# Kernel optimization log

Hardware: AMD Instinct MI355X
Metric: run time of the kernel (lower is better)

The kernel has to match this reference:

```python
import jax, jax.numpy as jnp
import numpy as np

B, S, D, L, H = 4, 2048, 1024, 2, 8  # batch, seq, d_model, hierarchy levels, heads
DH = D // H


def _ln(x, g, b, eps=1e-5):
    mu = jnp.mean(x, axis=-1, keepdims=True)
    xc = x - mu
    var = jnp.mean(xc * xc, axis=-1, keepdims=True)
    return xc * jax.lax.rsqrt(var + eps) * g + b


def setup_inputs() -> dict:
    key = jax.random.key(0)
    ks = jax.random.split(key, 16)
    s = 0.02
    f32 = jnp.float32
    return {
        "x": jax.random.normal(ks[0], (B, S, D), f32),
        "hierarchy_levels": jax.random.randint(ks[1], (B, S), 0, 3),
        # per-level processor MLPs (stacked over level axis)
        "p1_w": jax.random.normal(ks[2], (L, D, D), f32) * s,
        "p1_b": jnp.zeros((L, D), f32),
        "p2_w": jax.random.normal(ks[3], (L, D, D), f32) * s,
        "p2_b": jnp.zeros((L, D), f32),
        "ln_g": jnp.ones((L, D), f32),
        "ln_b": jnp.zeros((L, D), f32),
        # multihead attention projections
        "wq": jax.random.normal(ks[4], (D, D), f32) * s,
        "bq": jnp.zeros((D,), f32),
        "wk": jax.random.normal(ks[5], (D, D), f32) * s,
        "bk": jnp.zeros((D,), f32),
        "wv": jax.random.normal(ks[6], (D, D), f32) * s,
        "bv": jnp.zeros((D,), f32),
        "wo": jax.random.normal(ks[7], (D, D), f32) * s,
        "bo": jnp.zeros((D,), f32),
        # integration MLP: Linear(L*D -> D), SiLU, Linear(D -> D), LayerNorm
        "i1_w": jax.random.normal(ks[8], (L * D, D), f32) * s,
        "i1_b": jnp.zeros((D,), f32),
        "i2_w": jax.random.normal(ks[9], (D, D), f32) * s,
        "i2_b": jnp.zeros((D,), f32),
        "iln_g": jnp.ones((D,), f32),
        "iln_b": jnp.zeros((D,), f32),
    }


def reference(x, hierarchy_levels, p1_w, p1_b, p2_w, p2_b, ln_g, ln_b,
              wq, bq, wk, bk, wv, bv, wo, bo,
              i1_w, i1_b, i2_w, i2_b, iln_g, iln_b):
    # --- per-token expert routing: compute all L processors, select by level ---
    t = jax.nn.silu(jnp.einsum('bsd,lde->lbse', x, p1_w) + p1_b[:, None, None, :])
    h = jnp.einsum('lbse,led->lbsd', t, p2_w) + p2_b[:, None, None, :]
    h = _ln(h, ln_g[:, None, None, :], ln_b[:, None, None, :])  # [L,B,S,D]
    oh = jax.nn.one_hot(hierarchy_levels, L, dtype=x.dtype)      # [B,S,L]; level>=L -> all-zero row
    hsel = jnp.einsum('lbsd,bsl->bsd', h, oh)                    # [B,S,D]
    # --- self-attention over routed outputs ---
    q = (hsel @ wq + bq).reshape(B, S, H, DH)
    k = (hsel @ wk + bk).reshape(B, S, H, DH)
    v = (hsel @ wv + bv).reshape(B, S, H, DH)
    scores = jnp.einsum('bqhd,bkhd->bhqk', q, k) / np.sqrt(DH).astype(x.dtype)
    a = jax.nn.softmax(scores, axis=-1)                          # [B,H,S,S]
    ctx = jnp.einsum('bhqk,bkhd->bqhd', a, v).reshape(B, S, D)
    attended = ctx @ wo + bo
    attn_weights = jnp.mean(a, axis=1)                           # torch avg over heads: [B,S,S]
    # --- integration MLP ---
    z = jnp.concatenate([hsel, attended], axis=-1)               # [B,S,2D]
    z = jax.nn.silu(z @ i1_w + i1_b) @ i2_w + i2_b
    out = _ln(z, iln_g, iln_b)
    return out, attn_weights
```

## Files before the change

### kernel.cpp

```cpp
#include <hip/hip_runtime.h>
#include <cstdint>
#include <cstddef>

#define B_ 4
#define S_ 2048
#define D_ 1024
#define H_ 8
#define DH_ 128
#define MTOT 8192
#define NT_ 32
#define SCALE2 (0.08838834764831845f * 1.4426950408889634f)

typedef __attribute__((ext_vector_type(8))) short s16x8;
typedef __attribute__((ext_vector_type(4))) float f32x4;
typedef __attribute__((ext_vector_type(8))) __bf16 bf16x8;

static __device__ __forceinline__ f32x4 mfma16(s16x8 a, s16x8 b, f32x4 c) {
  return __builtin_amdgcn_mfma_f32_16x16x32_bf16(
      __builtin_bit_cast(bf16x8, a), __builtin_bit_cast(bf16x8, b), c, 0, 0, 0);
}
static __device__ __forceinline__ unsigned short f2bf(float f) {
  unsigned u = __builtin_bit_cast(unsigned, f);
  u += 0x7fffu + ((u >> 16) & 1u);
  return (unsigned short)(u >> 16);
}
static __device__ __forceinline__ float bf2f(unsigned short u) {
  return __builtin_bit_cast(float, (unsigned)u << 16);
}
static __device__ __forceinline__ unsigned cvtpk2(float a, float b) {
  unsigned r;
  asm("v_cvt_pk_bf16_f32 %0, %1, %2" : "=v"(r) : "v"(a), "v"(b));
  return r;
}
static __device__ __forceinline__ void gload_lds16(const void* g, void* l) {
  __builtin_amdgcn_global_load_lds(
      (__attribute__((address_space(1))) void*)(void*)(g),
      (__attribute__((address_space(3))) void*)(l), 16, 0, 0);
}

__global__ __launch_bounds__(256) void xconv_kernel(const float* __restrict__ x,
                                                    unsigned short* __restrict__ xb) {
  long i = ((long)blockIdx.x * 256 + threadIdx.x) * 4;
  float4 v = *(const float4*)(x + i);
  ushort4 o;
  o.x = f2bf(v.x); o.y = f2bf(v.y); o.z = f2bf(v.z); o.w = f2bf(v.w);
  *(ushort4*)(xb + i) = o;
}

__global__ __launch_bounds__(256) void route_kernel(const int* __restrict__ levels,
                                                    int* __restrict__ cnt,
                                                    int* __restrict__ ridx,
                                                    int* __restrict__ act,
                                                    int* __restrict__ act2) {
  const int row = blockIdx.x * 256 + threadIdx.x;
  const int lane = threadIdx.x & 63;
  const int lvl = levels[row];
  const unsigned long long lmlt = (lane == 63) ? ~0ULL >> 1 : (1ULL << lane) - 1;

#pragma unroll
  for (int c = 0; c < 2; c++) {
    bool pred = (lvl == c);
    unsigned long long mask = __ballot(pred);
    int total = __popcll(mask);
    if (total) {
      int leader = __ffsll((long long)mask) - 1;
      int base = 0;
      if (lane == leader) base = atomicAdd(&cnt[c], total);
      base = __shfl(base, leader);
      if (pred) ridx[c * MTOT + base + __popcll(mask & lmlt)] = row;
    }
  }
  {
    bool pred = (lvl < 2);
    unsigned long long mask = __ballot(pred);
    int total = __popcll(mask);
    if (total) {
      int leader = __ffsll((long long)mask) - 1;
      int base = 0;
      if (lane == leader) base = atomicAdd(&cnt[2], total);
      base = __shfl(base, leader);
      if (pred) act[base + __popcll(mask & lmlt)] = row;
    }
    unsigned long long mask2 = ~mask;
    int total2 = 64 - total;
    if (total2) {
      int leader2 = __ffsll((long long)mask2) - 1;
      int base2 = 0;
      if (lane == leader2) base2 = atomicAdd(&cnt[3], total2);
      base2 = __shfl(base2, leader2);
      if (!pred) act2[base2 + __popcll(mask2 & lmlt)] = row;
    }
  }
}

__global__ __launch_bounds__(256) void lvl2fill_kernel(
    const int* __restrict__ act2, const int* __restrict__ cntp,
    const float* __restrict__ bq, const float* __restrict__ bk,
    const float* __restrict__ bv,
    unsigned short* __restrict__ qb, unsigned short* __restrict__ kb,
    unsigned short* __restrict__ vb, unsigned short* __restrict__ z) {
  const int idx = blockIdx.x;
  if (idx >= *cntp) return;
  const long row = act2[idx];
  const int t = threadIdx.x;
  const float4 q4 = *(const float4*)(bq + t * 4);
  const float4 k4 = *(const float4*)(bk + t * 4);
  const float4 v4 = *(const float4*)(bv + t * 4);
  ushort4 qo, ko, vo;
  qo.x = f2bf(q4.x * SCALE2); qo.y = f2bf(q4.y * SCALE2);
  qo.z = f2bf(q4.z * SCALE2); qo.w = f2bf(q4.w * SCALE2);
  ko.x = f2bf(k4.x); ko.y = f2bf(k4.y); ko.z = f2bf(k4.z); ko.w = f2bf(k4.w);
  vo.x = f2bf(v4.x); vo.y = f2bf(v4.y); vo.z = f2bf(v4.z); vo.w = f2bf(v4.w);
  *(ushort4*)(qb + row * 1024 + t * 4) = qo;
  *(ushort4*)(kb + row * 1024 + t * 4) = ko;
  *(ushort4*)(vb + row * 1024 + t * 4) = vo;
  *(ushort4*)(z + row * 2048 + t * 4) = (ushort4){0, 0, 0, 0};
}

struct WtDesc { const float* src; unsigned short* dst; long dst_ld; long dst_off; };
struct WtArgs { WtDesc d[10]; };
__global__ __launch_bounds__(256) void wtrans_all_kernel(WtArgs a) {
  __shared__ unsigned short tile[32][33];
  const int wi = blockIdx.y >> 5;
  const WtDesc de = a.d[wi];
  int r0 = (blockIdx.y & 31) * 32, c0 = blockIdx.x * 32;
  int tr = threadIdx.x >> 5, tc = threadIdx.x & 31;
#pragma unroll
  for (int i = 0; i < 4; i++)
    tile[tr + i * 8][tc] = f2bf(de.src[(long)(r0 + tr + i * 8) * 1024 + c0 + tc]);
  __syncthreads();
#pragma unroll
  for (int i = 0; i < 4; i++)
    de.dst[(long)(c0 + tr + i * 8) * de.dst_ld + de.dst_off + r0 + tc] = tile[tc][tr + i * 8];
}

__global__ __launch_bounds__(256) void vtrans_kernel(const unsigned short* __restrict__ V,
                                                     unsigned short* __restrict__ Vt) {
  __shared__ unsigned short tile[32][33];
  int b = blockIdx.z;
  int h = blockIdx.y >> 2, d0 = (blockIdx.y & 3) * 32;
  int s0 = blockIdx.x * 32;
  int tr = threadIdx.x >> 5, tc = threadIdx.x & 31;
#pragma unroll
  for (int i = 0; i < 4; i++)
    tile[tr + i * 8][tc] = V[((long)(b * S_) + s0 + tr + i * 8) * D_ + h * DH_ + d0 + tc];
  __syncthreads();
  const int sk = s0 + tc;
  const int k6 = sk & 63;
  const int slot = ((k6 >> 5) << 5) | (((k6 >> 2) & 3) << 3) | (((k6 >> 4) & 1) << 2) | (k6 & 3);
  const int ss = (sk & ~63) | slot;
#pragma unroll
  for (int i = 0; i < 4; i++)
    Vt[((long)(b * H_ + h) * DH_ + d0 + tr + i * 8) * S_ + ss] = tile[tc][tr + i * 8];
}

template <int TAG>
__global__ __launch_bounds__(256) void gemm_kernel(
    const unsigned short* __restrict__ A, int lda,
    const unsigned short* __restrict__ Wt, int ldw,
    const float* __restrict__ bias, float oscale,
    unsigned short* __restrict__ Cb, float* __restrict__ Cf, int ldc,
    int K, int do_silu) {
  __shared__ unsigned short lA[128 * 64];
  __shared__ unsigned short lB[128 * 64];
  const int t = threadIdx.x;
  const int wid = t >> 6, lane = t & 63;
  const int g = lane >> 4, lc = lane & 15;
  const int wr = wid >> 1, wc = wid & 1;
  const int nwg = gridDim.x * gridDim.y;
  int flat = blockIdx.x + gridDim.x * blockIdx.y;
  flat = (flat & 7) * (nwg >> 3) + (flat >> 3);
  const int m0 = (flat / gridDim.x) * 128;
  const int n0 = (flat % gridDim.x) * 128;
  const int srow = lane >> 3, scol = lane & 7;
  const int sxor = (scol ^ srow) << 4;

  f32x4 acc[4][4];
#pragma unroll
  for (int i = 0; i < 4; i++)
#pragma unroll
    for (int j = 0; j < 4; j++) acc[i][j] = (f32x4){0.f, 0.f, 0.f, 0.f};

  const int nk = K >> 6;
  for (int kt = 0; kt < nk; ++kt) {
    const int k0 = kt << 6;
#pragma unroll
    for (int i = 0; i < 4; i++) {
      const int r0 = wid * 32 + i * 8;
      gload_lds16((const char*)(A + (m0 + r0 + srow) * (long)lda + k0) + sxor,
                  (char*)lA + r0 * 128);
      gload_lds16((const char*)(Wt + (n0 + r0 + srow) * (long)ldw + k0) + sxor,
                  (char*)lB + r0 * 128);
    }
    __syncthreads();
#pragma unroll
    for (int kk = 0; kk < 2; kk++) {
      s16x8 af[4], bfr[4];
#pragma unroll
      for (int i = 0; i < 4; i++) {
        int row = wr * 64 + i * 16 + lc;
        af[i] = *(const s16x8*)((const char*)lA + row * 128 +
                                ((kk * 64 + g * 16) ^ ((row & 7) << 4)));
      }
#pragma unroll
      for (int j = 0; j < 4; j++) {
        int row = wc * 64 + j * 16 + lc;
        bfr[j] = *(const s16x8*)((const char*)lB + row * 128 +
                                 ((kk * 64 + g * 16) ^ ((row & 7) << 4)));
      }
#pragma unroll
      for (int i = 0; i < 4; i++)
#pragma unroll
        for (int j = 0; j < 4; j++) acc[i][j] = mfma16(af[i], bfr[j], acc[i][j]);
    }
    __syncthreads();
  }
#pragma unroll
  for (int i = 0; i < 4; i++) {
    const long rbase = m0 + wr * 64 + i * 16 + g * 4;
#pragma unroll
    for (int j = 0; j < 4; j++) {
      const int col = n0 + wc * 64 + j * 16 + lc;
      const float bv = bias[col];
#pragma unroll
      for (int r = 0; r < 4; r++) {
        float v = (acc[i][j][r] + bv) * oscale;
        if (do_silu) v = v / (1.f + __expf(-v));
        if (Cb) Cb[(rbase + r) * (long)ldc + col] = f2bf(v);
        else Cf[(rbase + r) * (long)ldc + col] = v;
      }
    }
  }
}

template <int TAG>
__global__ __launch_bounds__(512) void gemm8_kernel(
    const unsigned short* __restrict__ A, int lda,
    const unsigned short* __restrict__ Wt, int ldw,
    const float* __restrict__ bias, float oscale,
    unsigned short* __restrict__ Cb, int ldc,
    int K, int do_silu) {
  __shared__ unsigned short lA[128 * 64];
  __shared__ unsigned short lB[128 * 64];
  const int t = threadIdx.x;
  const int wid = t >> 6, lane = t & 63;
  const int g = lane >> 4, lc = lane & 15;
  const int wr = wid >> 1, wc = wid & 1;
  const int nwg = gridDim.x * gridDim.y;
  int flat = blockIdx.x + gridDim.x * blockIdx.y;
  flat = (flat & 7) * (nwg >> 3) + (flat >> 3);
  const int m0 = (flat / gridDim.x) * 128;
  const int n0 = (flat % gridDim.x) * 128;
  const int srow = lane >> 3, scol = lane & 7;
  const int sxor = (scol ^ srow) << 4;

  f32x4 acc[2][4];
#pragma unroll
  for (int i = 0; i < 2; i++)
#pragma unroll
    for (int j = 0; j < 4; j++) acc[i][j] = (f32x4){0.f, 0.f, 0.f, 0.f};

  const int nk = K >> 6;
  for (int kt = 0; kt < nk; ++kt) {
    const int k0 = kt << 6;
#pragma unroll
    for (int i = 0; i < 2; i++) {
      const int r0 = wid * 16 + i * 8;
      gload_lds16((const char*)(A + (m0 + r0 + srow) * (long)lda + k0) + sxor,
                  (char*)lA + r0 * 128);
      gload_lds16((const char*)(Wt + (n0 + r0 + srow) * (long)ldw + k0) + sxor,
                  (char*)lB + r0 * 128);
    }
    __syncthreads();
#pragma unroll
    for (int kk = 0; kk < 2; kk++) {
      s16x8 af[2], bfr[4];
#pragma unroll
      for (int i = 0; i < 2; i++) {
        int row = wr * 32 + i * 16 + lc;
        af[i] = *(const s16x8*)((const char*)lA + row * 128 +
                                ((kk * 64 + g * 16) ^ ((row & 7) << 4)));
      }
#pragma unroll
      for (int j = 0; j < 4; j++) {
        int row = wc * 64 + j * 16 + lc;
        bfr[j] = *(const s16x8*)((const char*)lB + row * 128 +
                                 ((kk * 64 + g * 16) ^ ((row & 7) << 4)));
      }
#pragma unroll
      for (int i = 0; i < 2; i++)
#pragma unroll
        for (int j = 0; j < 4; j++) acc[i][j] = mfma16(af[i], bfr[j], acc[i][j]);
    }
    __syncthreads();
  }
#pragma unroll
  for (int i = 0; i < 2; i++) {
    const long rbase = m0 + wr * 32 + i * 16 + g * 4;
#pragma unroll
    for (int j = 0; j < 4; j++) {
      const int col = n0 + wc * 64 + j * 16 + lc;
      const float bv = bias[col];
#pragma unroll
      for (int r = 0; r < 4; r++) {
        float v = (acc[i][j][r] + bv) * oscale;
        if (do_silu) v = v / (1.f + __expf(-v));
        Cb[(rbase + r) * (long)ldc + col] = f2bf(v);
      }
    }
  }
}

template <int RMAP>
__global__ __launch_bounds__(512) void gemm8_moe_kernel(
    const unsigned short* __restrict__ A, int lda,
    const unsigned short* __restrict__ Wt0, int ldw,
    const float* __restrict__ bias0,
    unsigned short* __restrict__ Cb, int ldc,
    int K, int do_silu, const int* __restrict__ ridx, const int* __restrict__ cnt2) {
  __shared__ unsigned short lA[128 * 64];
  __shared__ unsigned short lB[128 * 64];
  const int t = threadIdx.x;
  const int wid = t >> 6, lane = t & 63;
  const int g = lane >> 4, lc = lane & 15;
  const int wr = wid >> 1, wc = wid & 1;
  const int nwg = gridDim.x * gridDim.y;
  int flat = blockIdx.x + gridDim.x * blockIdx.y;
  flat = (flat & 7) * (nwg >> 3) + (flat >> 3);
  const int m0 = (flat / gridDim.x) * 128;
  const int n0 = (flat % gridDim.x) * 128;
  const int lvl = m0 >> 12;
  const int lm0 = m0 & 4095;
  if (lm0 >= cnt2[lvl]) return;
  const unsigned short* Wt = Wt0 + (long)lvl * 1048576;
  const float* bias = bias0 + lvl * 1024;
  const int srow = lane >> 3, scol = lane & 7;
  const int sxor = (scol ^ srow) << 4;

  const unsigned short* abase[2];
#pragma unroll
  for (int i = 0; i < 2; i++) {
    int ar;
    if (RMAP) ar = ridx[lvl * MTOT + lm0 + wid * 16 + i * 8 + srow];
    else ar = m0 + wid * 16 + i * 8 + srow;
    abase[i] = A + (long)ar * lda;
  }

  f32x4 acc[2][4];
#pragma unroll
  for (int i = 0; i < 2; i++)
#pragma unroll
    for (int j = 0; j < 4; j++) acc[i][j] = (f32x4){0.f, 0.f, 0.f, 0.f};

  const int nk = K >> 6;
  for (int kt = 0; kt < nk; ++kt) {
    const int k0 = kt << 6;
#pragma unroll
    for (int i = 0; i < 2; i++) {
      const int r0 = wid * 16 + i * 8;
      gload_lds16((const char*)(abase[i] + k0) + sxor, (char*)lA + r0 * 128);
      gload_lds16((const char*)(Wt + (n0 + r0 + srow) * (long)ldw + k0) + sxor,
                  (char*)lB + r0 * 128);
    }
    __syncthreads();
#pragma unroll
    for (int kk = 0; kk < 2; kk++) {
      s16x8 af[2], bfr[4];
#pragma unroll
      for (int i = 0; i < 2; i++) {
        int row = wr * 32 + i * 16 + lc;
        af[i] = *(const s16x8*)((const char*)lA + row * 128 +
                                ((kk * 64 + g * 16) ^ ((row & 7) << 4)));
      }
#pragma unroll
      for (int j = 0; j < 4; j++) {
        int row = wc * 64 + j * 16 + lc;
        bfr[j] = *(const s16x8*)((const char*)lB + row * 128 +
                                 ((kk * 64 + g * 16) ^ ((row & 7) << 4)));
      }
#pragma unroll
      for (int i = 0; i < 2; i++)
#pragma unroll
        for (int j = 0; j < 4; j++) acc[i][j] = mfma16(af[i], bfr[j], acc[i][j]);
    }
    __syncthreads();
  }
#pragma unroll
  for (int i = 0; i < 2; i++) {
    const long rbase = m0 + wr * 32 + i * 16 + g * 4;
#pragma unroll
    for (int j = 0; j < 4; j++) {
      const int col = n0 + wc * 64 + j * 16 + lc;
      const float bv = bias[col];
#pragma unroll
      for (int r = 0; r < 4; r++) {
        float v = acc[i][j][r] + bv;
        if (do_silu) v = v / (1.f + __expf(-v));
        Cb[(rbase + r) * (long)ldc + col] = f2bf(v);
      }
    }
  }
}

__global__ __launch_bounds__(256) void wct_gemm_kernel(
    const unsigned short* __restrict__ A,
    const unsigned short* __restrict__ Wb,
    float* __restrict__ Cf) {
  __shared__ unsigned short lA[128 * 64];
  __shared__ unsigned short lB[128 * 64];
  const int t = threadIdx.x;
  const int wid = t >> 6, lane = t & 63;
  const int g = lane >> 4, lc = lane & 15;
  const int wr = wid >> 1, wc = wid & 1;
  const int chunk = blockIdx.y >> 3;
  const int m0 = (blockIdx.y & 7) * 128;
  const int n0 = blockIdx.x * 128;
  const unsigned short* A0 = A + chunk * 256;
  const unsigned short* W0 = Wb + chunk * 256;
  float* C0 = Cf + (long)chunk * 1048576;
  const int srow = lane >> 3, scol = lane & 7;
  const int sxor = (scol ^ srow) << 4;

  f32x4 acc[4][4];
#pragma unroll
  for (int i = 0; i < 4; i++)
#pragma unroll
    for (int j = 0; j < 4; j++) acc[i][j] = (f32x4){0.f, 0.f, 0.f, 0.f};

  for (int kt = 0; kt < 4; ++kt) {
    const int k0 = kt << 6;
#pragma unroll
    for (int i = 0; i < 4; i++) {
      const int r0 = wid * 32 + i * 8;
      gload_lds16((const char*)(A0 + (m0 + r0 + srow) * 2048L + k0) + sxor,
                  (char*)lA + r0 * 128);
      gload_lds16((const char*)(W0 + (n0 + r0 + srow) * 1024L + k0) + sxor,
                  (char*)lB + r0 * 128);
    }
    __syncthreads();
#pragma unroll
    for (int kk = 0; kk < 2; kk++) {
      s16x8 af[4], bfr[4];
#pragma unroll
      for (int i = 0; i < 4; i++) {
        int row = wr * 64 + i * 16 + lc;
        af[i] = *(const s16x8*)((const char*)lA + row * 128 +
                                ((kk * 64 + g * 16) ^ ((row & 7) << 4)));
      }
#pragma unroll
      for (int j = 0; j < 4; j++) {
        int row = wc * 64 + j * 16 + lc;
        bfr[j] = *(const s16x8*)((const char*)lB + row * 128 +
                                 ((kk * 64 + g * 16) ^ ((row & 7) << 4)));
      }
#pragma unroll
      for (int i = 0; i < 4; i++)
#pragma unroll
        for (int j = 0; j < 4; j++) acc[i][j] = mfma16(af[i], bfr[j], acc[i][j]);
    }
    __syncthreads();
  }
#pragma unroll
  for (int i = 0; i < 4; i++) {
    const long rbase = m0 + wr * 64 + i * 16 + g * 4;
#pragma unroll
    for (int j = 0; j < 4; j++) {
      const int col = n0 + wc * 64 + j * 16 + lc;
#pragma unroll
      for (int r = 0; r < 4; r++) C0[(rbase + r) * 1024L + col] = acc[i][j][r];
    }
  }
}

__global__ __launch_bounds__(256) void wct_reduce_kernel(
    const float* __restrict__ hraw, unsigned short* __restrict__ i1t) {
  long e = ((long)blockIdx.x * 256 + threadIdx.x) * 2;
  float a0 = hraw[e] + hraw[e + 1048576] + hraw[e + 2097152] + hraw[e + 3145728];
  float a1 = hraw[e + 1] + hraw[e + 1 + 1048576] + hraw[e + 1 + 2097152] +
             hraw[e + 1 + 3145728];
  unsigned pk = cvtpk2(a0, a1);
  long n = e >> 10, c = e & 1023;
  *(unsigned*)(i1t + n * 2048 + 1024 + c) = pk;
}

__global__ __launch_bounds__(256) void biascomb_kernel(
    const unsigned short* __restrict__ i1t, const float* __restrict__ bo,
    const float* __restrict__ i1b, float* __restrict__ bias_c) {
  const int n = blockIdx.x, t = threadIdx.x;
  ushort4 w = *(const ushort4*)(i1t + (long)n * 2048 + 1024 + t * 4);
  float4 b = *(const float4*)(bo + t * 4);
  float s = bf2f(w.x) * b.x + bf2f(w.y) * b.y + bf2f(w.z) * b.z + bf2f(w.w) * b.w;
#pragma unroll
  for (int m = 32; m; m >>= 1) s += __shfl_xor(s, m);
  __shared__ float ws_[4];
  if ((t & 63) == 0) ws_[t >> 6] = s;
  __syncthreads();
  if (t == 0) bias_c[n] = i1b[n] + ws_[0] + ws_[1] + ws_[2] + ws_[3];
}

__global__ __launch_bounds__(256) void ln_moe_kernel(
    const unsigned short* __restrict__ in, const int* __restrict__ ridx,
    const int* __restrict__ cnt2,
    const float* __restrict__ gg0, const float* __restrict__ bb0,
    unsigned short* __restrict__ outb, long ldo) {
  const int row = blockIdx.x;
  const int lvl = row >> 12;
  const int lrow = row & 4095;
  if (lrow >= cnt2[lvl]) return;
  const int orow = ridx[lvl * MTOT + lrow];
  const float* gg = gg0 + lvl * 1024;
  const float* bb = bb0 + lvl * 1024;
  const int t = threadIdx.x;
  const ushort4 u = *(const ushort4*)(in + (long)row * D_ + t * 4);
  float v0 = bf2f(u.x), v1 = bf2f(u.y), v2 = bf2f(u.z), v3 = bf2f(u.w);
  float s1 = v0 + v1 + v2 + v3;
  float s2 = v0 * v0 + v1 * v1 + v2 * v2 + v3 * v3;
#pragma unroll
  for (int m = 32; m; m >>= 1) {
    s1 += __shfl_xor(s1, m);
    s2 += __shfl_xor(s2, m);
  }
  __shared__ float w1[4], w2[4];
  if ((t & 63) == 0) { w1[t >> 6] = s1; w2[t >> 6] = s2; }
  __syncthreads();
  s1 = w1[0] + w1[1] + w1[2] + w1[3];
  s2 = w2[0] + w2[1] + w2[2] + w2[3];
  const float mu = s1 * (1.f / D_);
  const float var = s2 * (1.f / D_) - mu * mu;
  const float rs = rsqrtf(var + 1e-5f);
  float vv[4] = {v0, v1, v2, v3};
#pragma unroll
  for (int jj = 0; jj < 4; jj++) {
    int col = t * 4 + jj;
    float y = (vv[jj] - mu) * rs * gg[col] + bb[col];
    outb[(long)orow * ldo + col] = f2bf(y);
  }
}

__global__ __launch_bounds__(256) void ln_kernel(
    const unsigned short* __restrict__ in,
    const float* __restrict__ gg, const float* __restrict__ bb,
    float* __restrict__ outf) {
  const int row = blockIdx.x;
  const int t = threadIdx.x;
  const ushort4 u = *(const ushort4*)(in + (long)row * D_ + t * 4);
  float v0 = bf2f(u.x), v1 = bf2f(u.y), v2 = bf2f(u.z), v3 = bf2f(u.w);
  float s1 = v0 + v1 + v2 + v3;
  float s2 = v0 * v0 + v1 * v1 + v2 * v2 + v3 * v3;
#pragma unroll
  for (int m = 32; m; m >>= 1) {
    s1 += __shfl_xor(s1, m);
    s2 += __shfl_xor(s2, m);
  }
  __shared__ float w1[4], w2[4];
  if ((t & 63) == 0) { w1[t >> 6] = s1; w2[t >> 6] = s2; }
  __syncthreads();
  s1 = w1[0] + w1[1] + w1[2] + w1[3];
  s2 = w2[0] + w2[1] + w2[2] + w2[3];
  const float mu = s1 * (1.f / D_);
  const float var = s2 * (1.f / D_) - mu * mu;
  const float rs = rsqrtf(var + 1e-5f);
  float vv[4] = {v0, v1, v2, v3};
#pragma unroll
  for (int jj = 0; jj < 4; jj++) {
    int col = t * 4 + jj;
    outf[(long)row * D_ + col] = (vv[jj] - mu) * rs * gg[col] + bb[col];
  }
}

__global__ __launch_bounds__(256) void gemm_qkv_kernel(
    const unsigned short* __restrict__ A, int lda,
    const unsigned short* __restrict__ Wt,
    const float* __restrict__ bq, const float* __restrict__ bk,
    const float* __restrict__ bv,
    unsigned short* __restrict__ qb, unsigned short* __restrict__ kb,
    unsigned short* __restrict__ vb,
    const int* __restrict__ act, const int* __restrict__ cntp) {
  __shared__ unsigned short lA[128 * 64];
  __shared__ unsigned short lB[128 * 64];
  const int t = threadIdx.x;
  const int wid = t >> 6, lane = t & 63;
  const int g = lane >> 4, lc = lane & 15;
  const int wr = wid >> 1, wc = wid & 1;
  const int nwg = gridDim.x * gridDim.y;
  int flat = blockIdx.x + gridDim.x * blockIdx.y;
  flat = (flat & 7) * (nwg >> 3) + (flat >> 3);
  const int m0 = (flat / gridDim.x) * 128;
  const int n0 = (flat % gridDim.x) * 128;
  if (m0 >= *cntp) return;
  const int srow = lane >> 3, scol = lane & 7;
  const int sxor = (scol ^ srow) << 4;

  const unsigned short* abase[4];
#pragma unroll
  for (int i = 0; i < 4; i++)
    abase[i] = A + (long)act[m0 + wid * 32 + i * 8 + srow] * lda;

  f32x4 acc[4][4];
#pragma unroll
  for (int i = 0; i < 4; i++)
#pragma unroll
    for (int j = 0; j < 4; j++) acc[i][j] = (f32x4){0.f, 0.f, 0.f, 0.f};

  for (int kt = 0; kt < 16; ++kt) {
    const int k0 = kt << 6;
#pragma unroll
    for (int i = 0; i < 4; i++) {
      const int r0 = wid * 32 + i * 8;
      gload_lds16((const char*)(abase[i] + k0) + sxor, (char*)lA + r0 * 128);
      gload_lds16((const char*)(Wt + (n0 + r0 + srow) * 1024 + k0) + sxor,
                  (char*)lB + r0 * 128);
    }
    __syncthreads();
#pragma unroll
    for (int kk = 0; kk < 2; kk++) {
      s16x8 af[4], bfr[4];
#pragma unroll
      for (int i = 0; i < 4; i++) {
        int row = wr * 64 + i * 16 + lc;
        af[i] = *(const s16x8*)((const char*)lA + row * 128 +
                                ((kk * 64 + g * 16) ^ ((row & 7) << 4)));
      }
#pragma unroll
      for (int j = 0; j < 4; j++) {
        int row = wc * 64 + j * 16 + lc;
        bfr[j] = *(const s16x8*)((const char*)lB + row * 128 +
                                 ((kk * 64 + g * 16) ^ ((row & 7) << 4)));
      }
#pragma unroll
      for (int i = 0; i < 4; i++)
#pragma unroll
        for (int j = 0; j < 4; j++) acc[i][j] = mfma16(af[i], bfr[j], acc[i][j]);
    }
    __syncthreads();
  }
  const int whichB = n0 >> 10;
  const float* bias = whichB == 0 ? bq : whichB == 1 ? bk : bv;
  unsigned short* Cb = whichB == 0 ? qb : whichB == 1 ? kb : vb;
  const float oscale = whichB == 0 ? (float)SCALE2 : 1.0f;
  const int nb = n0 & 1023;
#pragma unroll
  for (int i = 0; i < 4; i++) {
    const int ribase = m0 + wr * 64 + i * 16 + g * 4;
#pragma unroll
    for (int j = 0; j < 4; j++) {
      const int col = nb + wc * 64 + j * 16 + lc;
      const float bvv = bias[col];
#pragma unroll
      for (int r = 0; r < 4; r++) {
        float v = (acc[i][j][r] + bvv) * oscale;
        Cb[(long)act[ribase + r] * 1024L + col] = f2bf(v);
      }
    }
  }
}

__global__ __launch_bounds__(256, 2) void flash_kernel(
    const unsigned short* __restrict__ Q, const unsigned short* __restrict__ Kb,
    const unsigned short* __restrict__ Vt,
    unsigned short* __restrict__ zatt, float* __restrict__ Mo, float* __restrict__ Lo) {
  __shared__ unsigned short lK[2][64 * 128];
  __shared__ unsigned short lV[2][128 * 64];
  const int t = threadIdx.x, wid = t >> 6, lane = t & 63;
  const int g = lane >> 4, lc = lane & 15;
  const int d = blockIdx.x + 16 * (blockIdx.y + 8 * blockIdx.z);
  const int qd = d >> 3, rd = d & 7;
  const int grp = rd + 8 * (qd >> 4);
  const int b = grp >> 3, h = grp & 7, q0 = (qd & 15) * 128;
  const int k_l4 = lane >> 4, k_c = lane & 15;
  const int v_l3 = lane >> 3, v_c = lane & 7;

  s16x8 qf[2][4];
#pragma unroll
  for (int qi = 0; qi < 2; qi++)
#pragma unroll
    for (int kk = 0; kk < 4; kk++)
      qf[qi][kk] = *(const s16x8*)(Q +
          ((long)(b * S_ + q0 + wid * 32 + qi * 16 + lc)) * D_ + h * DH_ + kk * 32 + g * 8);

  f32x4 acco[2][8];
#pragma unroll
  for (int qi = 0; qi < 2; qi++)
#pragma unroll
    for (int dn = 0; dn < 8; dn++) acco[qi][dn] = (f32x4){0.f, 0.f, 0.f, 0.f};
  float m_run[2] = {-1e30f, -1e30f}, l_run[2] = {0.f, 0.f};

  auto stageK = [&](int kt, int buf) {
#pragma unroll
    for (int i = 0; i < 4; i++) {
      const int r0 = wid * 16 + i * 4;
      const int row = r0 + k_l4;
      gload_lds16((const char*)(Kb + (b * S_ + kt * 64 + row) * D_ + h * DH_) +
                      ((k_c ^ (row & 7)) << 4),
                  (char*)&lK[buf][0] + r0 * 256);
    }
  };
  auto stageV = [&](int kt, int buf) {
#pragma unroll
    for (int i = 0; i < 4; i++) {
      const int r0 = wid * 32 + i * 8;
      const int row = r0 + v_l3;
      gload_lds16((const char*)(Vt + ((b * H_ + h) * DH_ + row) * S_ + kt * 64) +
                      ((v_c ^ (row & 7)) << 4),
                  (char*)&lV[buf][0] + r0 * 128);
    }
  };

  stageK(0, 0);
  stageV(0, 0);
  __syncthreads();

  for (int kt = 0; kt < NT_; ++kt) {
    const int cur = kt & 1;
    if (kt + 1 < NT_) { stageK(kt + 1, cur ^ 1); stageV(kt + 1, cur ^ 1); }

    f32x4 s[2][4];
#pragma unroll
    for (int qi = 0; qi < 2; qi++)
#pragma unroll
      for (int kn = 0; kn < 4; kn++) s[qi][kn] = (f32x4){0.f, 0.f, 0.f, 0.f};
    __builtin_amdgcn_s_setprio(1);
#pragma unroll
    for (int kk = 0; kk < 4; kk++) {
      s16x8 kf[4];
#pragma unroll
      for (int kn = 0; kn < 4; kn++) {
        int row = kn * 16 + lc;
        kf[kn] = *(const s16x8*)((const char*)&lK[cur][0] + row * 256 +
                                 ((kk * 64 + g * 16) ^ ((row & 7) << 4)));
      }
#pragma unroll
      for (int qi = 0; qi < 2; qi++)
#pragma unroll
        for (int kn = 0; kn < 4; kn++) s[qi][kn] = mfma16(kf[kn], qf[qi][kk], s[qi][kn]);
    }
    __builtin_amdgcn_s_setprio(0);

    float mx[2];
    int trig = 0;
#pragma unroll
    for (int qi = 0; qi < 2; qi++) {
      float m01 = fmaxf(fmaxf(s[qi][0][0], s[qi][0][1]), fmaxf(s[qi][0][2], s[qi][0][3]));
      float m1 = fmaxf(fmaxf(s[qi][1][0], s[qi][1][1]), fmaxf(s[qi][1][2], s[qi][1][3]));
      float m2 = fmaxf(fmaxf(s[qi][2][0], s[qi][2][1]), fmaxf(s[qi][2][2], s[qi][2][3]));
      float m3 = fmaxf(fmaxf(s[qi][3][0], s[qi][3][1]), fmaxf(s[qi][3][2], s[qi][3][3]));
      float m = fmaxf(fmaxf(m01, m1), fmaxf(m2, m3));
      m = fmaxf(m, __shfl_xor(m, 16));
      m = fmaxf(m, __shfl_xor(m, 32));
      mx[qi] = m;
      trig |= (m > m_run[qi] + 8.0f);
    }
    if (__any(trig)) {
#pragma unroll
      for (int qi = 0; qi < 2; qi++) {
        float mn = fmaxf(m_run[qi], mx[qi]);
        float fsc = exp2f(m_run[qi] - mn);
        m_run[qi] = mn;
        l_run[qi] *= fsc;
#pragma unroll
        for (int dn = 0; dn < 8; dn++)
#pragma unroll
          for (int r = 0; r < 4; r++) acco[qi][dn][r] *= fsc;
      }
    }

    unsigned w[2][4][2];
#pragma unroll
    for (int qi = 0; qi < 2; qi++) {
      float ls = 0.f;
#pragma unroll
      for (int kn = 0; kn < 4; kn++) {
        float p0 = exp2f(s[qi][kn][0] - m_run[qi]);
        float p1 = exp2f(s[qi][kn][1] - m_run[qi]);
        float p2 = exp2f(s[qi][kn][2] - m_run[qi]);
        float p3 = exp2f(s[qi][kn][3] - m_run[qi]);
        ls += (p0 + p1) + (p2 + p3);
        w[qi][kn][0] = cvtpk2(p0, p1);
        w[qi][kn][1] = cvtpk2(p2, p3);
      }
      ls += __shfl_xor(ls, 16);
      ls += __shfl_xor(ls, 32);
      l_run[qi] += ls;
    }

    __builtin_amdgcn_s_setprio(1);
#pragma unroll
    for (int kk = 0; kk < 2; kk++) {
      s16x8 pf[2];
#pragma unroll
      for (int qi = 0; qi < 2; qi++) {
        union { unsigned u[4]; s16x8 v; } pu;
        pu.u[0] = w[qi][2 * kk][0];
        pu.u[1] = w[qi][2 * kk][1];
        pu.u[2] = w[qi][2 * kk + 1][0];
        pu.u[3] = w[qi][2 * kk + 1][1];
        pf[qi] = pu.v;
      }
#pragma unroll
      for (int dn = 0; dn < 8; dn++) {
        int vrow = dn * 16 + lc;
        s16x8 vf = *(const s16x8*)((const char*)&lV[cur][0] + vrow * 128 +
                                   ((kk * 64 + g * 16) ^ ((vrow & 7) << 4)));
#pragma unroll
        for (int qi = 0; qi < 2; qi++) acco[qi][dn] = mfma16(vf, pf[qi], acco[qi][dn]);
      }
    }
    __builtin_amdgcn_s_setprio(0);
    __syncthreads();
  }

  char* tb = (char*)&lK[0][0] + wid * 8192;
#pragma unroll
  for (int qi = 0; qi < 2; qi++) {
    float inv = 1.f / l_run[qi];
    int row = qi * 16 + lc;
#pragma unroll
    for (int dn = 0; dn < 8; dn++) {
      unsigned lo = cvtpk2(acco[qi][dn][0] * inv, acco[qi][dn][1] * inv);
      unsigned hi = cvtpk2(acco[qi][dn][2] * inv, acco[qi][dn][3] * inv);
      unsigned long long pk = (unsigned long long)lo | ((unsigned long long)hi << 32);
      *(unsigned long long*)(tb + row * 256 + ((dn * 32 + g * 8) ^ ((row & 7) << 4))) = pk;
    }
  }
  __syncthreads();
#pragma unroll
  for (int i = 0; i < 8; i++) {
    const int row = i * 4 + (lane >> 4);
    const int chunk = lane & 15;
    s16x8 vv = *(const s16x8*)(tb + row * 256 + ((chunk * 16) ^ ((row & 7) << 4)));
    *(s16x8*)(zatt + ((long)(b * S_ + q0 + wid * 32 + row)) * 2048 + h * DH_ + chunk * 8) = vv;
  }
  if (g == 0) {
#pragma unroll
    for (int qi = 0; qi < 2; qi++) {
      int q = q0 + wid * 32 + qi * 16 + lc;
      Mo[(long)(b * H_ + h) * S_ + q] = m_run[qi];
      Lo[(long)(b * H_ + h) * S_ + q] = l_run[qi];
    }
  }
}

__global__ __launch_bounds__(256) void attw_kernel(
    const unsigned short* __restrict__ Q, const unsigned short* __restrict__ Kb,
    const float* __restrict__ Mo, const float* __restrict__ Lo,
    float* __restrict__ AW) {
  __shared__ unsigned short lK[2][128 * 128];
  __shared__ float lm[H_][128], winv[H_][128];
  const int t = threadIdx.x, wid = t >> 6, lane = t & 63;
  const int g = lane >> 4, lc = lane & 15;
  const int f = blockIdx.x + 16 * (blockIdx.y + 16 * blockIdx.z);
  const int xcd = f & 7, i_ = f >> 3;
  const int grp = (i_ >> 4) * 8 + xcd;
  const int b = grp >> 4, k0 = (grp & 15) * 128, q0 = (i_ & 15) * 128;
  const int k_l4 = lane >> 4, k_c = lane & 15;

  for (int i = t; i < H_ * 128; i += 256) {
    int h = i >> 7, qq = i & 127;
    lm[h][qq] = Mo[(long)(b * H_ + h) * S_ + q0 + qq];
    winv[h][qq] = 0.125f / Lo[(long)(b * H_ + h) * S_ + q0 + qq];
  }

  auto stageK = [&](int h, int buf) {
#pragma unroll
    for (int i = 0; i < 8; i++) {
      const int r0 = wid * 32 + i * 4;
      const int row = r0 + k_l4;
      gload_lds16((const char*)(Kb + ((long)(b * S_ + k0 + row)) * D_ + h * DH_) +
                      ((k_c ^ (row & 7)) << 4),
                  (char*)&lK[buf][0] + r0 * 256);
    }
  };

  f32x4 acc[2][8];
#pragma unroll
  for (int qi = 0; qi < 2; qi++)
#pragma unroll
    for (int kn = 0; kn < 8; kn++) acc[qi][kn] = (f32x4){0.f, 0.f, 0.f, 0.f};

  stageK(0, 0);
  __syncthreads();

  for (int h = 0; h < H_; ++h) {
    const int cur = h & 1;
    if (h + 1 < H_) stageK(h + 1, cur ^ 1);
    f32x4 s[2][8];
#pragma unroll
    for (int qi = 0; qi < 2; qi++)
#pragma unroll
      for (int kn = 0; kn < 8; kn++) s[qi][kn] = (f32x4){0.f, 0.f, 0.f, 0.f};
    __builtin_amdgcn_s_setprio(1);
#pragma unroll
    for (int kk = 0; kk < 4; kk++) {
      s16x8 qa[2];
#pragma unroll
      for (int qi = 0; qi < 2; qi++)
        qa[qi] = *(const s16x8*)(Q +
            ((long)(b * S_ + q0 + wid * 32 + qi * 16 + lc)) * D_ + h * DH_ + kk * 32 + g * 8);
#pragma unroll
      for (int kn = 0; kn < 8; kn++) {
        int row = kn * 16 + lc;
        s16x8 kf = *(const s16x8*)((const char*)&lK[cur][0] + row * 256 +
                                   ((kk * 64 + g * 16) ^ ((row & 7) << 4)));
#pragma unroll
        for (int qi = 0; qi < 2; qi++) s[qi][kn] = mfma16(qa[qi], kf, s[qi][kn]);
      }
    }
    __builtin_amdgcn_s_setprio(0);
#pragma unroll
    for (int qi = 0; qi < 2; qi++)
#pragma unroll
      for (int kn = 0; kn < 8; kn++)
#pragma unroll
        for (int r = 0; r < 4; r++) {
          int qq = wid * 32 + qi * 16 + g * 4 + r;
          acc[qi][kn][r] += exp2f(s[qi][kn][r] - lm[h][qq]) * winv[h][qq];
        }
    __syncthreads();
  }
#pragma unroll
  for (int qi = 0; qi < 2; qi++)
#pragma unroll
    for (int kn = 0; kn < 8; kn++)
#pragma unroll
      for (int r = 0; r < 4; r++) {
        long q = q0 + wid * 32 + qi * 16 + g * 4 + r;
        int k = k0 + kn * 16 + lc;
        AW[((long)b * S_ + q) * S_ + k] = acc[qi][kn][r];
      }
}

__global__ void signal_kernel(float* out, float v) { out[0] = v; }

extern "C" void kernel_launch(void* const* d_in, const int* in_sizes, int n_in,
                              void* d_out, int out_size, void* d_ws, size_t ws_size,
                              hipStream_t stream) {
  constexpr size_t OFF_XB = 0;
  constexpr size_t OFF_W = 16777216ULL;
  constexpr size_t OFF_T = 39845888ULL;
  constexpr size_t OFF_HR = 56623104ULL;
  constexpr size_t OFF_Z = 90177536ULL;
  constexpr size_t OFF_Q = 123731968ULL;
  constexpr size_t OFF_K = 140509184ULL;
  constexpr size_t OFF_V = 157286400ULL;
  constexpr size_t OFF_VT = 174063616ULL;
  constexpr size_t OFF_M = 190840832ULL;
  constexpr size_t OFF_L = 191102976ULL;
  constexpr size_t OFF_CNT = 191365120ULL;
  constexpr size_t OFF_RIDX = 191365184ULL;
  constexpr size_t OFF_BC = OFF_RIDX + 2ULL * MTOT * 4;
  constexpr size_t OFF_ACT = OFF_BC + 4096;
  constexpr size_t OFF_ACT2 = OFF_ACT + MTOT * 4;
  constexpr size_t WS_NEED = OFF_ACT2 + MTOT * 4;

  if (ws_size < WS_NEED) {
    signal_kernel<<<1, 1, 0, stream>>>((float*)d_out, (float)ws_size);
    return;
  }
  const float* x = (const float*)d_in[0];
  const int* levels = (const int*)d_in[1];
  const float* p1w = (const float*)d_in[2];
  const float* p1b = (const float*)d_in[3];
  const float* p2w = (const float*)d_in[4];
  const float* p2b = (const float*)d_in[5];
  const float* lng = (const float*)d_in[6];
  const float* lnb = (const float*)d_in[7];
  const float* wq = (const float*)d_in[8];
  const float* bq = (const float*)d_in[9];
  const float* wk = (const float*)d_in[10];
  const float* bk = (const float*)d_in[11];
  const float* wv = (const float*)d_in[12];
  const float* bv = (const float*)d_in[13];
  const float* wo = (const float*)d_in[14];
  const float* bo = (const float*)d_in[15];
  const float* i1w = (const float*)d_in[16];
  const float* i1b = (const float*)d_in[17];
  const float* i2w = (const float*)d_in[18];
  const float* i2b = (const float*)d_in[19];
  const float* ilng = (const float*)d_in[20];
  const float* ilnb = (const float*)d_in[21];

  char* ws = (char*)d_ws;
  unsigned short* xb = (unsigned short*)(ws + OFF_XB);
  unsigned short* p1t = (unsigned short*)(ws + OFF_W);
  unsigned short* p2t = p1t + 2 * 1048576;
  unsigned short* wqt = p2t + 2 * 1048576;
  unsigned short* wkt = wqt + 1048576;
  unsigned short* wvt = wkt + 1048576;
  unsigned short* wob = wvt + 1048576;
  unsigned short* i1t = wob + 1048576;
  unsigned short* i2t = i1t + 2097152;
  unsigned short* tbuf = (unsigned short*)(ws + OFF_T);
  float* wctp = (float*)(ws + OFF_HR);
  unsigned short* hraw16 = (unsigned short*)(ws + OFF_HR);
  unsigned short* z = (unsigned short*)(ws + OFF_Z);
  unsigned short* qb = (unsigned short*)(ws + OFF_Q);
  unsigned short* kb = (unsigned short*)(ws + OFF_K);
  unsigned short* vb = (unsigned short*)(ws + OFF_V);
  unsigned short* vt = (unsigned short*)(ws + OFF_VT);
  float* Mo = (float*)(ws + OFF_M);
  float* Lo = (float*)(ws + OFF_L);
  int* cnt = (int*)(ws + OFF_CNT);
  int* ridx = (int*)(ws + OFF_RIDX);
  float* bias_c = (float*)(ws + OFF_BC);
  int* act = (int*)(ws + OFF_ACT);
  int* act2 = (int*)(ws + OFF_ACT2);
  float* out = (float*)d_out;
  float* aw = out + (size_t)MTOT * D_;

  dim3 blk(256), blk8(512);
  hipMemsetAsync(cnt, 0, 64, stream);
  hipMemsetAsync(ridx, 0, 2 * MTOT * 4, stream);
  hipMemsetAsync(act, 0, MTOT * 4, stream);
  xconv_kernel<<<8192, blk, 0, stream>>>(x, xb);
  route_kernel<<<32, blk, 0, stream>>>(levels, cnt, ridx, act, act2);
  lvl2fill_kernel<<<MTOT, blk, 0, stream>>>(act2, cnt + 3, bq, bk, bv, qb, kb, vb, z);

  WtArgs wa;
  wa.d[0] = {p1w, p1t, 1024, 0};
  wa.d[1] = {p1w + 1048576, p1t + 1048576, 1024, 0};
  wa.d[2] = {p2w, p2t, 1024, 0};
  wa.d[3] = {p2w + 1048576, p2t + 1048576, 1024, 0};
  wa.d[4] = {wq, wqt, 1024, 0};
  wa.d[5] = {wk, wkt, 1024, 0};
  wa.d[6] = {wv, wvt, 1024, 0};
  wa.d[7] = {i1w, i1t, 2048, 0};
  wa.d[8] = {i1w + 1048576, i1t, 2048, 1024};
  wa.d[9] = {i2w, i2t, 1024, 0};
  wtrans_all_kernel<<<dim3(32, 320), blk, 0, stream>>>(wa);
  xconv_kernel<<<1024, blk, 0, stream>>>(wo, wob);
  wct_gemm_kernel<<<dim3(8, 32), blk, 0, stream>>>(i1t + 1024, wob, wctp);
  biascomb_kernel<<<1024, blk, 0, stream>>>(i1t, bo, i1b, bias_c);
  wct_reduce_kernel<<<2048, blk, 0, stream>>>(wctp, i1t);

  gemm8_moe_kernel<1><<<dim3(8, 64), blk8, 0, stream>>>(xb, 1024, p1t, 1024, p1b,
                                                        tbuf, 1024, 1024, 1, ridx, cnt);
  gemm8_moe_kernel<0><<<dim3(8, 64), blk8, 0, stream>>>(tbuf, 1024, p2t, 1024, p2b,
                                                        hraw16, 1024, 1024, 0, ridx, cnt);
  ln_moe_kernel<<<8192, blk, 0, stream>>>(hraw16, ridx, cnt, lng, lnb, z, 2048);

  gemm_qkv_kernel<<<dim3(24, 64), blk, 0, stream>>>(z, 2048, wqt, bq, bk, bv, qb, kb, vb,
                                                    act, cnt + 2);
  vtrans_kernel<<<dim3(64, 32, 4), blk, 0, stream>>>(vb, vt);
  flash_kernel<<<dim3(16, 8, 4), blk, 0, stream>>>(qb, kb, vt, z + 1024, Mo, Lo);
  attw_kernel<<<dim3(16, 16, 4), blk, 0, stream>>>(qb, kb, Mo, Lo, aw);
  gemm8_kernel<3><<<dim3(8, 64), blk8, 0, stream>>>(z, 2048, i1t, 2048, bias_c, 1.0f, tbuf,
                                                    1024, 2048, 1);
  gemm8_kernel<4><<<dim3(8, 64), blk8, 0, stream>>>(tbuf, 1024, i2t, 1024, i2b, 1.0f, hraw16,
                                                    1024, 1024, 0);
  ln_kernel<<<8192, blk, 0, stream>>>(hraw16, ilng, ilnb, out);
}
```

Before: 440.7 us.

## Skip integration MLP for unrouted rows and broadcast per-batch representative output

Tokens whose level is at least L get an all-zero hsel. Their q/k/v reduce to the biases, so every such token in a batch gets the same attended vector and the same final output. The integration GEMMs and LayerNorm now run only on routed rows plus one representative unrouted row per batch, gathered through an index list. A broadcast kernel then copies the representative output to the other unrouted rows. The wo bf16 conversion is also folded into the x conversion launch, which saves one kernel launch at the cost of an extra small prep kernel and a broadcast pass.

```diff
diff --git a/kernel.cpp b/kernel.cpp
--- a/kernel.cpp
+++ b/kernel.cpp
@@ -38,13 +38,23 @@
       (__attribute__((address_space(3))) void*)(l), 16, 0, 0);
 }
 
-__global__ __launch_bounds__(256) void xconv_kernel(const float* __restrict__ x,
-                                                    unsigned short* __restrict__ xb) {
-  long i = ((long)blockIdx.x * 256 + threadIdx.x) * 4;
-  float4 v = *(const float4*)(x + i);
-  ushort4 o;
-  o.x = f2bf(v.x); o.y = f2bf(v.y); o.z = f2bf(v.z); o.w = f2bf(v.w);
-  *(ushort4*)(xb + i) = o;
+__global__ __launch_bounds__(256) void xconv2_kernel(const float* __restrict__ x,
+                                                     unsigned short* __restrict__ xb,
+                                                     const float* __restrict__ wo,
+                                                     unsigned short* __restrict__ wob) {
+  if (blockIdx.x < 8192) {
+    long i = ((long)blockIdx.x * 256 + threadIdx.x) * 4;
+    float4 v = *(const float4*)(x + i);
+    ushort4 o;
+    o.x = f2bf(v.x); o.y = f2bf(v.y); o.z = f2bf(v.z); o.w = f2bf(v.w);
+    *(ushort4*)(xb + i) = o;
+  } else {
+    long i = ((long)(blockIdx.x - 8192) * 256 + threadIdx.x) * 4;
+    float4 v = *(const float4*)(wo + i);
+    ushort4 o;
+    o.x = f2bf(v.x); o.y = f2bf(v.y); o.z = f2bf(v.z); o.w = f2bf(v.w);
+    *(ushort4*)(wob + i) = o;
+  }
 }
 
 __global__ __launch_bounds__(256) void route_kernel(const int* __restrict__ levels,
@@ -90,6 +100,30 @@
       base2 = __shfl(base2, leader2);
       if (!pred) act2[base2 + __popcll(mask2 & lmlt)] = row;
     }
+  }
+}
+
+__global__ __launch_bounds__(256) void prep2_kernel(int* __restrict__ cnt,
+                                                    const int* __restrict__ act2,
+                                                    int* __restrict__ act,
+                                                    int* __restrict__ rep) {
+  const int t = threadIdx.x;
+  __shared__ int srep[4];
+  if (t < 4) srep[t] = -1;
+  __syncthreads();
+  const int n3 = cnt[3];
+  for (int i = t; i < n3; i += 256) {
+    int row = act2[i];
+    srep[row >> 11] = row;
+  }
+  __syncthreads();
+  if (t == 0) {
+    int c = cnt[2];
+    for (int b = 0; b < 4; b++) {
+      rep[b] = srep[b];
+      if (srep[b] >= 0) act[c++] = srep[b];
+    }
+    cnt[8] = c;
   }
 }
 
@@ -117,6 +151,19 @@
   *(ushort4*)(z + row * 2048 + t * 4) = (ushort4){0, 0, 0, 0};
 }
 
+__global__ __launch_bounds__(256) void bcast_out_kernel(
+    const int* __restrict__ act2, const int* __restrict__ cntp,
+    const int* __restrict__ rep, float* __restrict__ out) {
+  const int idx = blockIdx.x;
+  if (idx >= *cntp) return;
+  const long row = act2[idx];
+  const int b = (int)(row >> 11);
+  const long rp = rep[b];
+  if (row == rp) return;
+  const int t = threadIdx.x;
+  *(float4*)(out + row * 1024 + t * 4) = *(const float4*)(out + rp * 1024 + t * 4);
+}
+
 struct WtDesc { const float* src; unsigned short* dst; long dst_ld; long dst_off; };
 struct WtArgs { WtDesc d[10]; };
 __global__ __launch_bounds__(256) void wtrans_all_kernel(WtArgs a) {
@@ -154,13 +201,13 @@
     Vt[((long)(b * H_ + h) * DH_ + d0 + tr + i * 8) * S_ + ss] = tile[tc][tr + i * 8];
 }
 
-template <int TAG>
-__global__ __launch_bounds__(256) void gemm_kernel(
+template <int GATHER>
+__global__ __launch_bounds__(512) void gemm8_route_kernel(
     const unsigned short* __restrict__ A, int lda,
     const unsigned short* __restrict__ Wt, int ldw,
-    const float* __restrict__ bias, float oscale,
-    unsigned short* __restrict__ Cb, float* __restrict__ Cf, int ldc,
-    int K, int do_silu) {
+    const float* __restrict__ bias,
+    unsigned short* __restrict__ Cb, int ldc,
+    int K, int do_silu, const int* __restrict__ list, const int* __restrict__ cntp) {
   __shared__ unsigned short lA[128 * 64];
   __shared__ unsigned short lB[128 * 64];
   const int t = threadIdx.x;
@@ -172,12 +219,21 @@
   flat = (flat & 7) * (nwg >> 3) + (flat >> 3);
   const int m0 = (flat / gridDim.x) * 128;
   const int n0 = (flat % gridDim.x) * 128;
+  if (cntp && m0 >= *cntp) return;
   const int srow = lane >> 3, scol = lane & 7;
   const int sxor = (scol ^ srow) << 4;
 
-  f32x4 acc[4][4];
-#pragma unroll
-  for (int i = 0; i < 4; i++)
+  const unsigned short* abase[2];
+#pragma unroll
+  for (int i = 0; i < 2; i++) {
+    int ar = m0 + wid * 16 + i * 8 + srow;
+    if (GATHER) ar = list[ar];
+    abase[i] = A + (long)ar * lda;
+  }
+
+  f32x4 acc[2][4];
+#pragma unroll
+  for (int i = 0; i < 2; i++)
 #pragma unroll
     for (int j = 0; j < 4; j++) acc[i][j] = (f32x4){0.f, 0.f, 0.f, 0.f};
 
@@ -185,20 +241,19 @@
   for (int kt = 0; kt < nk; ++kt) {
     const int k0 = kt << 6;
 #pragma unroll
-    for (int i = 0; i < 4; i++) {
-      const int r0 = wid * 32 + i * 8;
-      gload_lds16((const char*)(A + (m0 + r0 + srow) * (long)lda + k0) + sxor,
-                  (char*)lA + r0 * 128);
+    for (int i = 0; i < 2; i++) {
+      const int r0 = wid * 16 + i * 8;
+      gload_lds16((const char*)(abase[i] + k0) + sxor, (char*)lA + r0 * 128);
       gload_lds16((const char*)(Wt + (n0 + r0 + srow) * (long)ldw + k0) + sxor,
                   (char*)lB + r0 * 128);
     }
     __syncthreads();
 #pragma unroll
     for (int kk = 0; kk < 2; kk++) {
-      s16x8 af[4], bfr[4];
-#pragma unroll
-      for (int i = 0; i < 4; i++) {
-        int row = wr * 64 + i * 16 + lc;
+      s16x8 af[2], bfr[4];
+#pragma unroll
+      for (int i = 0; i < 2; i++) {
+        int row = wr * 32 + i * 16 + lc;
         af[i] = *(const s16x8*)((const char*)lA + row * 128 +
                                 ((kk * 64 + g * 16) ^ ((row & 7) << 4)));
       }
@@ -209,101 +264,22 @@
                                  ((kk * 64 + g * 16) ^ ((row & 7) << 4)));
       }
 #pragma unroll
-      for (int i = 0; i < 4; i++)
+      for (int i = 0; i < 2; i++)
 #pragma unroll
         for (int j = 0; j < 4; j++) acc[i][j] = mfma16(af[i], bfr[j], acc[i][j]);
     }
     __syncthreads();
   }
 #pragma unroll
-  for (int i = 0; i < 4; i++) {
-    const long rbase = m0 + wr * 64 + i * 16 + g * 4;
+  for (int i = 0; i < 2; i++) {
+    const long rbase = m0 + wr * 32 + i * 16 + g * 4;
 #pragma unroll
     for (int j = 0; j < 4; j++) {
       const int col = n0 + wc * 64 + j * 16 + lc;
       const float bv = bias[col];
 #pragma unroll
       for (int r = 0; r < 4; r++) {
-        float v = (acc[i][j][r] + bv) * oscale;
-        if (do_silu) v = v / (1.f + __expf(-v));
-        if (Cb) Cb[(rbase + r) * (long)ldc + col] = f2bf(v);
-        else Cf[(rbase + r) * (long)ldc + col] = v;
-      }
-    }
-  }
-}
-
-template <int TAG>
-__global__ __launch_bounds__(512) void gemm8_kernel(
-    const unsigned short* __restrict__ A, int lda,
-    const unsigned short* __restrict__ Wt, int ldw,
-    const float* __restrict__ bias, float oscale,
-    unsigned short* __restrict__ Cb, int ldc,
-    int K, int do_silu) {
-  __shared__ unsigned short lA[128 * 64];
-  __shared__ unsigned short lB[128 * 64];
-  const int t = threadIdx.x;
-  const int wid = t >> 6, lane = t & 63;
-  const int g = lane >> 4, lc = lane & 15;
-  const int wr = wid >> 1, wc = wid & 1;
-  const int nwg = gridDim.x * gridDim.y;
-  int flat = blockIdx.x + gridDim.x * blockIdx.y;
-  flat = (flat & 7) * (nwg >> 3) + (flat >> 3);
-  const int m0 = (flat / gridDim.x) * 128;
-  const int n0 = (flat % gridDim.x) * 128;
-  const int srow = lane >> 3, scol = lane & 7;
-  const int sxor = (scol ^ srow) << 4;
-
-  f32x4 acc[2][4];
-#pragma unroll
-  for (int i = 0; i < 2; i++)
-#pragma unroll
-    for (int j = 0; j < 4; j++) acc[i][j] = (f32x4){0.f, 0.f, 0.f, 0.f};
-
-  const int nk = K >> 6;
-  for (int kt = 0; kt < nk; ++kt) {
-    const int k0 = kt << 6;
-#pragma unroll
-    for (int i = 0; i < 2; i++) {
-      const int r0 = wid * 16 + i * 8;
-      gload_lds16((const char*)(A + (m0 + r0 + srow) * (long)lda + k0) + sxor,
-                  (char*)lA + r0 * 128);
-      gload_lds16((const char*)(Wt + (n0 + r0 + srow) * (long)ldw + k0) + sxor,
-                  (char*)lB + r0 * 128);
-    }
-    __syncthreads();
-#pragma unroll
-    for (int kk = 0; kk < 2; kk++) {
-      s16x8 af[2], bfr[4];
-#pragma unroll
-      for (int i = 0; i < 2; i++) {
-        int row = wr * 32 + i * 16 + lc;
-        af[i] = *(const s16x8*)((const char*)lA + row * 128 +
-                                ((kk * 64 + g * 16) ^ ((row & 7) << 4)));
-      }
-#pragma unroll
-      for (int j = 0; j < 4; j++) {
-        int row = wc * 64 + j * 16 + lc;
-        bfr[j] = *(const s16x8*)((const char*)lB + row * 128 +
-                                 ((kk * 64 + g * 16) ^ ((row & 7) << 4)));
-      }
-#pragma unroll
-      for (int i = 0; i < 2; i++)
-#pragma unroll
-        for (int j = 0; j < 4; j++) acc[i][j] = mfma16(af[i], bfr[j], acc[i][j]);
-    }
-    __syncthreads();
-  }
-#pragma unroll
-  for (int i = 0; i < 2; i++) {
-    const long rbase = m0 + wr * 32 + i * 16 + g * 4;
-#pragma unroll
-    for (int j = 0; j < 4; j++) {
-      const int col = n0 + wc * 64 + j * 16 + lc;
-      const float bv = bias[col];
-#pragma unroll
-      for (int r = 0; r < 4; r++) {
-        float v = (acc[i][j][r] + bv) * oscale;
+        float v = acc[i][j][r] + bv;
         if (do_silu) v = v / (1.f + __expf(-v));
         Cb[(rbase + r) * (long)ldc + col] = f2bf(v);
       }
@@ -538,10 +514,13 @@
 }
 
 __global__ __launch_bounds__(256) void ln_kernel(
-    const unsigned short* __restrict__ in,
+    const unsigned short* __restrict__ in, const int* __restrict__ list,
+    const int* __restrict__ cntp,
     const float* __restrict__ gg, const float* __restrict__ bb,
     float* __restrict__ outf) {
   const int row = blockIdx.x;
+  if (row >= *cntp) return;
+  const int orow = list[row];
   const int t = threadIdx.x;
   const ushort4 u = *(const ushort4*)(in + (long)row * D_ + t * 4);
   float v0 = bf2f(u.x), v1 = bf2f(u.y), v2 = bf2f(u.z), v3 = bf2f(u.w);
@@ -564,7 +543,7 @@
 #pragma unroll
   for (int jj = 0; jj < 4; jj++) {
     int col = t * 4 + jj;
-    outf[(long)row * D_ + col] = (vv[jj] - mu) * rs * gg[col] + bb[col];
+    outf[(long)orow * D_ + col] = (vv[jj] - mu) * rs * gg[col] + bb[col];
   }
 }
 
@@ -950,7 +929,8 @@
   constexpr size_t OFF_BC = OFF_RIDX + 2ULL * MTOT * 4;
   constexpr size_t OFF_ACT = OFF_BC + 4096;
   constexpr size_t OFF_ACT2 = OFF_ACT + MTOT * 4;
-  constexpr size_t WS_NEED = OFF_ACT2 + MTOT * 4;
+  constexpr size_t OFF_REP = OFF_ACT2 + MTOT * 4;
+  constexpr size_t WS_NEED = OFF_REP + 64;
 
   if (ws_size < WS_NEED) {
     signal_kernel<<<1, 1, 0, stream>>>((float*)d_out, (float)ws_size);
@@ -1004,6 +984,7 @@
   float* bias_c = (float*)(ws + OFF_BC);
   int* act = (int*)(ws + OFF_ACT);
   int* act2 = (int*)(ws + OFF_ACT2);
+  int* rep = (int*)(ws + OFF_REP);
   float* out = (float*)d_out;
   float* aw = out + (size_t)MTOT * D_;
 
@@ -1011,8 +992,9 @@
   hipMemsetAsync(cnt, 0, 64, stream);
   hipMemsetAsync(ridx, 0, 2 * MTOT * 4, stream);
   hipMemsetAsync(act, 0, MTOT * 4, stream);
-  xconv_kernel<<<8192, blk, 0, stream>>>(x, xb);
+  xconv2_kernel<<<9216, blk, 0, stream>>>(x, xb, wo, wob);
   route_kernel<<<32, blk, 0, stream>>>(levels, cnt, ridx, act, act2);
+  prep2_kernel<<<1, blk, 0, stream>>>(cnt, act2, act, rep);
   lvl2fill_kernel<<<MTOT, blk, 0, stream>>>(act2, cnt + 3, bq, bk, bv, qb, kb, vb, z);
 
   WtArgs wa;
@@ -1027,7 +1009,6 @@
   wa.d[8] = {i1w + 1048576, i1t, 2048, 1024};
   wa.d[9] = {i2w, i2t, 1024, 0};
   wtrans_all_kernel<<<dim3(32, 320), blk, 0, stream>>>(wa);
-  xconv_kernel<<<1024, blk, 0, stream>>>(wo, wob);
   wct_gemm_kernel<<<dim3(8, 32), blk, 0, stream>>>(i1t + 1024, wob, wctp);
   biascomb_kernel<<<1024, blk, 0, stream>>>(i1t, bo, i1b, bias_c);
   wct_reduce_kernel<<<2048, blk, 0, stream>>>(wctp, i1t);
@@ -1043,9 +1024,12 @@
   vtrans_kernel<<<dim3(64, 32, 4), blk, 0, stream>>>(vb, vt);
   flash_kernel<<<dim3(16, 8, 4), blk, 0, stream>>>(qb, kb, vt, z + 1024, Mo, Lo);
   attw_kernel<<<dim3(16, 16, 4), blk, 0, stream>>>(qb, kb, Mo, Lo, aw);
-  gemm8_kernel<3><<<dim3(8, 64), blk8, 0, stream>>>(z, 2048, i1t, 2048, bias_c, 1.0f, tbuf,
-                                                    1024, 2048, 1);
-  gemm8_kernel<4><<<dim3(8, 64), blk8, 0, stream>>>(tbuf, 1024, i2t, 1024, i2b, 1.0f, hraw16,
-                                                    1024, 1024, 0);
-  ln_kernel<<<8192, blk, 0, stream>>>(hraw16, ilng, ilnb, out);
-}
+
+  gemm8_route_kernel<1><<<dim3(8, 64), blk8, 0, stream>>>(z, 2048, i1t, 2048, bias_c,
+                                                          tbuf, 1024, 2048, 1, act, cnt + 8);
+  gemm8_route_kernel<0><<<dim3(8, 64), blk8, 0, stream>>>(tbuf, 1024, i2t, 1024, i2b,
+                                                          hraw16, 1024, 1024, 0, nullptr,
+                                                          cnt + 8);
+  ln_kernel<<<8192, blk, 0, stream>>>(hraw16, act, cnt + 8, ilng, ilnb, out);
+  bcast_out_kernel<<<MTOT, blk, 0, stream>>>(act2, cnt + 3, rep, out);
+}
```

Measured after the change: 447.6 us. Within noise of the previous version (+1.6%).
